# Kernel optimization log

Measured on AMD Instinct MI355X. Metric: run time of the kernel, lower is better.

The kernel has to match this reference:

```python
import jax, jax.numpy as jnp
import numpy as np

D_MODEL = 1024
NUM_HEADS = 16
D_K = D_MODEL // NUM_HEADS
CLAMP = 1e9
EPS = 1e-12


def setup_inputs() -> dict:
    key = jax.random.key(0)
    ks = jax.random.split(key, 11)
    B, S, D = 4, 2048, D_MODEL
    std = 1.0 / np.sqrt(D)
    inp = {
        'Q': jax.random.normal(ks[0], (B, S, D), jnp.float32),
        'K': jax.random.normal(ks[1], (B, S, D), jnp.float32),
        'V': jax.random.normal(ks[2], (B, S, D), jnp.float32),
        'Wq': jax.random.normal(ks[3], (D, D), jnp.float32) * std,
        'bq': jnp.zeros((D,), jnp.float32),
        'Wk': jax.random.normal(ks[4], (D, D), jnp.float32) * std,
        'bk': jnp.zeros((D,), jnp.float32),
        'Wv': jax.random.normal(ks[5], (D, D), jnp.float32) * std,
        'bv': jnp.zeros((D,), jnp.float32),
        'Wo': jax.random.normal(ks[6], (D, D), jnp.float32) * std,
        'bo': jnp.zeros((D,), jnp.float32),
    }
    return inp


def _split_heads(x):
    b, s, _ = x.shape
    return x.reshape(b, s, NUM_HEADS, D_K).transpose(0, 2, 1, 3)  # [b,h,s,dk]


def reference(Q, K, V, Wq, bq, Wk, bk, Wv, bv, Wo, bo):
    Qh = _split_heads(Q @ Wq.T + bq)
    Kh = _split_heads(K @ Wk.T + bk)
    Vh = _split_heads(V @ Wv.T + bv)
    scale = jnp.sqrt(jnp.asarray(D_K, Qh.dtype))
    scores = jnp.einsum('bhqd,bhkd->bhqk', Qh, Kh) / scale
    scores = scores - jnp.max(scores, axis=-1, keepdims=True)
    scores = jnp.clip(scores, -CLAMP, CLAMP)
    attn = jax.nn.softmax(scores, axis=-1)
    attn = jnp.clip(attn, EPS, None)
    attn = attn / jnp.sum(attn, axis=-1, keepdims=True)
    ctx = jnp.einsum('bhqk,bhkd->bhqd', attn, Vh)
    b, h, s, dk = ctx.shape
    ctx = ctx.transpose(0, 2, 1, 3).reshape(b, s, D_MODEL)
    return ctx @ Wo.T + bo
```

## Files before the change

kernel.cpp:

```cpp
#include <hip/hip_runtime.h>
#include <hip/hip_bf16.h>


typedef float  f32x4  __attribute__((ext_vector_type(4)));
typedef __bf16 bf16x8 __attribute__((ext_vector_type(8)));
typedef short  s16x8  __attribute__((ext_vector_type(8)));
typedef int    i32x4  __attribute__((ext_vector_type(4)));

#define MFMA16(a,b,c) __builtin_amdgcn_mfma_f32_16x16x32_bf16((a),(b),(c),0,0,0)

__device__ __forceinline__ unsigned short f2bf(float f) {
    union { float f; unsigned u; } v; v.f = f;
    unsigned r = v.u + 0x7fffu + ((v.u >> 16) & 1u);
    return (unsigned short)(r >> 16);
}

__device__ __forceinline__ s16x8 cvt8(const float* __restrict__ p) {
    f32x4 x = *(const f32x4*)p;
    f32x4 y = *(const f32x4*)(p + 4);
    s16x8 r;
    r[0] = (short)f2bf(x[0]); r[1] = (short)f2bf(x[1]);
    r[2] = (short)f2bf(x[2]); r[3] = (short)f2bf(x[3]);
    r[4] = (short)f2bf(y[0]); r[5] = (short)f2bf(y[1]);
    r[6] = (short)f2bf(y[2]); r[7] = (short)f2bf(y[3]);
    return r;
}

__device__ __forceinline__ void gl_lds16(const void* g, void* l) {
    __builtin_amdgcn_global_load_lds(
        (const __attribute__((address_space(1))) unsigned int*)g,
        (__attribute__((address_space(3))) unsigned int*)l, 16, 0, 0);
}

__device__ __forceinline__ float exp2_fast(float x) {
    float r;
    asm("v_exp_f32 %0, %1" : "=v"(r) : "v"(x));
    return r;
}

__device__ __forceinline__ int cvtpk_bf16(float lo, float hi) {
    int r;
    asm("v_cvt_pk_bf16_f32 %0, %1, %2" : "=v"(r) : "v"(lo), "v"(hi));
    return r;
}
__device__ __forceinline__ void plswap32(int& a, int& b) {
    asm("v_permlane32_swap_b32 %0, %1" : "+v"(a), "+v"(b));
}
__device__ __forceinline__ void plswap16(int& a, int& b) {
    asm("v_permlane16_swap_b32 %0, %1" : "+v"(a), "+v"(b));
}

__device__ __forceinline__ void pack_pf(const f32x4 pe[4], bf16x8& pf0, bf16x8& pf1) {
    int a0 = cvtpk_bf16(pe[0][0], pe[0][1]);
    int a1 = cvtpk_bf16(pe[0][2], pe[0][3]);
    int b0 = cvtpk_bf16(pe[1][0], pe[1][1]);
    int b1 = cvtpk_bf16(pe[1][2], pe[1][3]);
    plswap32(a0, b0); plswap32(a1, b1);
    plswap16(a0, b0); plswap16(a1, b1);
    i32x4 f0; f0[0] = a0; f0[1] = a1; f0[2] = b0; f0[3] = b1;
    int c0 = cvtpk_bf16(pe[2][0], pe[2][1]);
    int c1 = cvtpk_bf16(pe[2][2], pe[2][3]);
    int d0 = cvtpk_bf16(pe[3][0], pe[3][1]);
    int d1 = cvtpk_bf16(pe[3][2], pe[3][3]);
    plswap32(c0, d0); plswap32(c1, d1);
    plswap16(c0, d0); plswap16(c1, d1);
    i32x4 f1; f1[0] = c0; f1[1] = c1; f1[2] = d0; f1[3] = d1;
    pf0 = __builtin_bit_cast(bf16x8, f0);
    pf1 = __builtin_bit_cast(bf16x8, f1);
}

__global__ __launch_bounds__(256) void cvt_kernel(
    const float* __restrict__ src, unsigned short* __restrict__ dst, int n8)
{
    int i = blockIdx.x * 256 + threadIdx.x;
    if (i < n8) *(s16x8*)(dst + (size_t)i * 8) = cvt8(src + (size_t)i * 8);
}

template <int MODE>
__global__ __launch_bounds__(256) void gemm_bf16(
    const unsigned short* __restrict__ A,
    const unsigned short* __restrict__ W,
    const float* __restrict__ bias,
    void* __restrict__ Cv, float scale)
{
    constexpr int K = 1024;
    __shared__ unsigned short Ash[128 * 32];
    __shared__ unsigned short Bsh[128 * 32];

    const int t    = threadIdx.x;
    const int w    = t >> 6;
    const int lane = t & 63;
    const int wm   = w >> 1, wn = w & 1;
    const int lr   = lane & 15, quad = lane >> 4;

    const int m0 = blockIdx.y * 128;
    const int n0 = blockIdx.x * 128;

    const int srow = t >> 2;
    const int skp  = (t & 3) * 8;

    const unsigned short* Ap0 = A + (size_t)(m0 + srow) * K + skp;
    const unsigned short* Ap1 = Ap0 + (size_t)64 * K;
    const unsigned short* Wp0 = W + (size_t)(n0 + srow) * K + skp;
    const unsigned short* Wp1 = Wp0 + (size_t)64 * K;
    unsigned short* lA0 = &Ash[w * 512];
    unsigned short* lA1 = &Ash[2048 + w * 512];
    unsigned short* lB0 = &Bsh[w * 512];
    unsigned short* lB1 = &Bsh[2048 + w * 512];

    f32x4 acc[4][4] = {};

    for (int k0 = 0; k0 < K; k0 += 32) {
        __syncthreads();
        gl_lds16(Ap0 + k0, lA0);
        gl_lds16(Ap1 + k0, lA1);
        gl_lds16(Wp0 + k0, lB0);
        gl_lds16(Wp1 + k0, lB1);
        __syncthreads();

        bf16x8 af[4], bw[4];
#pragma unroll
        for (int i = 0; i < 4; i++)
            af[i] = *(const bf16x8*)&Ash[(wm * 64 + i * 16 + lr) * 32 + quad * 8];
#pragma unroll
        for (int j = 0; j < 4; j++)
            bw[j] = *(const bf16x8*)&Bsh[(wn * 64 + j * 16 + lr) * 32 + quad * 8];

#pragma unroll
        for (int i = 0; i < 4; i++)
#pragma unroll
            for (int j = 0; j < 4; j++)
                acc[i][j] = MFMA16(af[i], bw[j], acc[i][j]);
    }

#pragma unroll
    for (int i = 0; i < 4; i++) {
#pragma unroll
        for (int j = 0; j < 4; j++) {
            const int n = n0 + wn * 64 + j * 16 + lr;
#pragma unroll
            for (int r = 0; r < 4; r++) {
                const int m = m0 + wm * 64 + i * 16 + quad * 4 + r;
                float val = (acc[i][j][r] + ((MODE == 2) ? bias[m] : bias[n])) * scale;
                if (MODE == 0) {
                    const int b = m >> 11, s = m & 2047, h = n >> 6, d = n & 63;
                    ((unsigned short*)Cv)[(((size_t)(b * 16 + h) * 2048 + s) << 6) + d] = f2bf(val);
                } else if (MODE == 1) {
                    ((float*)Cv)[(size_t)m * 1024 + n] = val;
                } else {
                    const int h = m >> 6, d = m & 63, b = n >> 11, s = n & 2047;
                    ((unsigned short*)Cv)[((size_t)(b * 16 + h) * 64 + d) * 2048 + s] = f2bf(val);
                }
            }
        }
    }
}

__global__ __launch_bounds__(256) void attn_kernel(
    const unsigned short* __restrict__ Qh,
    const unsigned short* __restrict__ Kh,
    const unsigned short* __restrict__ Vt,
    unsigned short* __restrict__ ctx)
{
    constexpr int KS = 72;
    __shared__ unsigned short Ksh[64 * KS];
    __shared__ unsigned short Vts[64 * KS];

    const int t    = threadIdx.x;
    const int w    = t >> 6;
    const int lane = t & 63;
    const int lr   = lane & 15, quad = lane >> 4;

    const int bh = blockIdx.y, qblk = blockIdx.x;
    const size_t base = (size_t)bh * 2048 * 64;
    const unsigned short* Qp = Qh + base;
    const unsigned short* Kg = Kh + base + (size_t)lane * 64 + w * 16;
    const unsigned short* Vg = Vt + base + (size_t)lane * 2048 + w * 16;

    const int q0 = qblk * 128 + w * 32;
    const unsigned short* qr0 = Qp + (size_t)(q0 + lr) * 64;
    const unsigned short* qr1 = Qp + (size_t)(q0 + 16 + lr) * 64;
    bf16x8 aq0 = *(const bf16x8*)(qr0 + quad * 8);
    bf16x8 aq1 = *(const bf16x8*)(qr0 + 32 + quad * 8);
    bf16x8 aq2 = *(const bf16x8*)(qr1 + quad * 8);
    bf16x8 aq3 = *(const bf16x8*)(qr1 + 32 + quad * 8);

    f32x4 Of0[4] = {}, Of1[4] = {};
    float ls0 = 0.f, ls1 = 0.f;

    s16x8 kv0 = *(const s16x8*)(Kg);
    s16x8 kv1 = *(const s16x8*)(Kg + 8);
    s16x8 vv0 = *(const s16x8*)(Vg);
    s16x8 vv1 = *(const s16x8*)(Vg + 8);

    for (int kb = 0; kb < 2048; kb += 64) {
        __syncthreads();
        *(s16x8*)&Ksh[lane * KS + w * 16]     = kv0;
        *(s16x8*)&Ksh[lane * KS + w * 16 + 8] = kv1;
        *(s16x8*)&Vts[lane * KS + w * 16]     = vv0;
        *(s16x8*)&Vts[lane * KS + w * 16 + 8] = vv1;

        const int kn = (kb + 64) & 2047;
        kv0 = *(const s16x8*)(Kg + (size_t)kn * 64);
        kv1 = *(const s16x8*)(Kg + (size_t)kn * 64 + 8);
        vv0 = *(const s16x8*)(Vg + kn);
        vv1 = *(const s16x8*)(Vg + kn + 8);

        __syncthreads();

        f32x4 pe0[4], pe1[4];
#pragma unroll
        for (int nt = 0; nt < 4; nt++) {
            const unsigned short* kr = &Ksh[(16 * nt + lr) * KS + quad * 8];
            bf16x8 k0 = *(const bf16x8*)kr;
            bf16x8 k1 = *(const bf16x8*)(kr + 32);
            f32x4 c0 = {}, c1 = {};
            c0 = MFMA16(k0, aq0, c0); c0 = MFMA16(k1, aq1, c0);
            c1 = MFMA16(k0, aq2, c1); c1 = MFMA16(k1, aq3, c1);
            f32x4 p0, p1;
#pragma unroll
            for (int r = 0; r < 4; r++) p0[r] = exp2_fast(c0[r]);
#pragma unroll
            for (int r = 0; r < 4; r++) p1[r] = exp2_fast(c1[r]);
            ls0 += (p0[0] + p0[1]) + (p0[2] + p0[3]);
            ls1 += (p1[0] + p1[1]) + (p1[2] + p1[3]);
            pe0[nt] = p0; pe1[nt] = p1;
        }

        bf16x8 pf00, pf01, pf10, pf11;
        pack_pf(pe0, pf00, pf01);
        pack_pf(pe1, pf10, pf11);

#pragma unroll
        for (int dt = 0; dt < 4; dt++) {
            const unsigned short* vr = &Vts[(dt * 16 + lr) * KS + quad * 8];
            bf16x8 v0 = *(const bf16x8*)vr;
            bf16x8 v1 = *(const bf16x8*)(vr + 32);
            Of0[dt] = MFMA16(pf00, v0, Of0[dt]);
            Of0[dt] = MFMA16(pf01, v1, Of0[dt]);
            Of1[dt] = MFMA16(pf10, v0, Of1[dt]);
            Of1[dt] = MFMA16(pf11, v1, Of1[dt]);
        }
    }

    ls0 += __shfl_xor(ls0, 16);
    ls0 += __shfl_xor(ls0, 32);
    ls1 += __shfl_xor(ls1, 16);
    ls1 += __shfl_xor(ls1, 32);

    const int b = bh >> 4, h = bh & 15;
#pragma unroll
    for (int r = 0; r < 4; r++) {
        const float inv0 = 1.0f / __shfl(ls0, quad * 4 + r, 64);
        const int qa = q0 + quad * 4 + r;
        unsigned short* cp0 = ctx + ((size_t)b * 2048 + qa) * 1024 + h * 64;
#pragma unroll
        for (int dt = 0; dt < 4; dt++)
            cp0[dt * 16 + lr] = f2bf(Of0[dt][r] * inv0);

        const float inv1 = 1.0f / __shfl(ls1, quad * 4 + r, 64);
        const int qb = q0 + 16 + quad * 4 + r;
        unsigned short* cp1 = ctx + ((size_t)b * 2048 + qb) * 1024 + h * 64;
#pragma unroll
        for (int dt = 0; dt < 4; dt++)
            cp1[dt * 16 + lr] = f2bf(Of1[dt][r] * inv1);
    }
}

extern "C" void kernel_launch(void* const* d_in, const int* in_sizes, int n_in,
                              void* d_out, int out_size, void* d_ws, size_t ws_size,
                              hipStream_t stream) {
    const float* Q  = (const float*)d_in[0];
    const float* K  = (const float*)d_in[1];
    const float* V  = (const float*)d_in[2];
    const float* Wq = (const float*)d_in[3];
    const float* bq = (const float*)d_in[4];
    const float* Wk = (const float*)d_in[5];
    const float* bk = (const float*)d_in[6];
    const float* Wv = (const float*)d_in[7];
    const float* bv = (const float*)d_in[8];
    const float* Wo = (const float*)d_in[9];
    const float* bo = (const float*)d_in[10];

    const size_t EB = (size_t)8192 * 1024;
    const size_t EW = (size_t)1024 * 1024;
    unsigned short* Xb  = (unsigned short*)d_ws;
    unsigned short* Wqb = Xb  + EB;
    unsigned short* Wkb = Wqb + EW;
    unsigned short* Wvb = Wkb + EW;
    unsigned short* Wob = Wvb + EW;
    unsigned short* Qh  = Wob + EW;
    unsigned short* Kh  = Qh  + EB;
    unsigned short* Vtw = Kh  + EB;
    unsigned short* Ctx = Xb;

    const int n8b = (int)(EB / 8);
    const int n8w = (int)(EW / 8);

    const float QSCALE = 0.125f * 1.44269504088896340736f;

    cvt_kernel<<<n8w / 256, 256, 0, stream>>>(Wq, Wqb, n8w);
    cvt_kernel<<<n8w / 256, 256, 0, stream>>>(Wk, Wkb, n8w);
    cvt_kernel<<<n8w / 256, 256, 0, stream>>>(Wv, Wvb, n8w);
    cvt_kernel<<<n8w / 256, 256, 0, stream>>>(Wo, Wob, n8w);

    dim3 tb(256), gP(8, 64), gT(64, 8);

    cvt_kernel<<<n8b / 256, 256, 0, stream>>>(Q, Xb, n8b);
    gemm_bf16<0><<<gP, tb, 0, stream>>>(Xb, Wqb, bq, Qh, QSCALE);

    cvt_kernel<<<n8b / 256, 256, 0, stream>>>(K, Xb, n8b);
    gemm_bf16<0><<<gP, tb, 0, stream>>>(Xb, Wkb, bk, Kh, 1.0f);

    cvt_kernel<<<n8b / 256, 256, 0, stream>>>(V, Xb, n8b);
    gemm_bf16<2><<<gT, tb, 0, stream>>>(Wvb, Xb, bv, Vtw, 1.0f);

    attn_kernel<<<dim3(16, 64), tb, 0, stream>>>(Qh, Kh, Vtw, Ctx);

    gemm_bf16<1><<<gP, tb, 0, stream>>>(Ctx, Wob, bo, (float*)d_out, 1.0f);
}
```

Baseline: 373.0 us.

## Double-buffer GEMM LDS tiles, remap block order, fuse weight conversions

The GEMM now double-buffers its LDS tiles. It issues the next k-slice's global-to-LDS loads before computing the current one and waits with explicit vmcnt counts, so the load of one slice overlaps the MFMAs of the previous one. For the non-transposed modes, the block index is remapped so consecutive blocks share the same N-column of weights, which should help L2 reuse. The four weight-conversion launches are merged into one kernel. LDS use per block doubles, which may reduce occupancy, and correctness depends on the hand-written waitcnt and barrier placement.

```diff
diff --git a/kernel.cpp b/kernel.cpp
--- a/kernel.cpp
+++ b/kernel.cpp
@@ -76,6 +76,19 @@
     if (i < n8) *(s16x8*)(dst + (size_t)i * 8) = cvt8(src + (size_t)i * 8);
 }
 
+__global__ __launch_bounds__(256) void wcvt_kernel(
+    const float* __restrict__ s0, const float* __restrict__ s1,
+    const float* __restrict__ s2, const float* __restrict__ s3,
+    unsigned short* __restrict__ d0, unsigned short* __restrict__ d1,
+    unsigned short* __restrict__ d2, unsigned short* __restrict__ d3)
+{
+    const int which = blockIdx.x >> 9;
+    const int i = (blockIdx.x & 511) * 256 + threadIdx.x;
+    const float* s = (which == 0) ? s0 : (which == 1) ? s1 : (which == 2) ? s2 : s3;
+    unsigned short* d = (which == 0) ? d0 : (which == 1) ? d1 : (which == 2) ? d2 : d3;
+    *(s16x8*)(d + (size_t)i * 8) = cvt8(s + (size_t)i * 8);
+}
+
 template <int MODE>
 __global__ __launch_bounds__(256) void gemm_bf16(
     const unsigned short* __restrict__ A,
@@ -84,8 +97,8 @@
     void* __restrict__ Cv, float scale)
 {
     constexpr int K = 1024;
-    __shared__ unsigned short Ash[128 * 32];
-    __shared__ unsigned short Bsh[128 * 32];
+    __shared__ unsigned short Ash[2 * 128 * 32];
+    __shared__ unsigned short Bsh[2 * 128 * 32];
 
     const int t    = threadIdx.x;
     const int w    = t >> 6;
@@ -93,8 +106,16 @@
     const int wm   = w >> 1, wn = w & 1;
     const int lr   = lane & 15, quad = lane >> 4;
 
-    const int m0 = blockIdx.y * 128;
-    const int n0 = blockIdx.x * 128;
+    int m0, n0;
+    if (MODE == 2) {
+        m0 = blockIdx.y * 128;
+        n0 = blockIdx.x * 128;
+    } else {
+        const int bid  = blockIdx.y * 8 + blockIdx.x;
+        const int orig = (bid & 7) * 64 + (bid >> 3);
+        n0 = (orig & 7) * 128;
+        m0 = (orig >> 3) * 128;
+    }
 
     const int srow = t >> 2;
     const int skp  = (t & 3) * 8;
@@ -108,30 +129,47 @@
     unsigned short* lB0 = &Bsh[w * 512];
     unsigned short* lB1 = &Bsh[2048 + w * 512];
 
+#define STAGE(buf, k0) do {                       \
+        gl_lds16(Ap0 + (k0), lA0 + (buf) * 4096); \
+        gl_lds16(Ap1 + (k0), lA1 + (buf) * 4096); \
+        gl_lds16(Wp0 + (k0), lB0 + (buf) * 4096); \
+        gl_lds16(Wp1 + (k0), lB1 + (buf) * 4096); \
+    } while (0)
+
     f32x4 acc[4][4] = {};
 
+    STAGE(0, 0);
+    int cur = 0;
+
     for (int k0 = 0; k0 < K; k0 += 32) {
-        __syncthreads();
-        gl_lds16(Ap0 + k0, lA0);
-        gl_lds16(Ap1 + k0, lA1);
-        gl_lds16(Wp0 + k0, lB0);
-        gl_lds16(Wp1 + k0, lB1);
-        __syncthreads();
+        if (k0 + 32 < K) {
+            STAGE(cur ^ 1, k0 + 32);
+            asm volatile("s_waitcnt vmcnt(4)" ::: "memory");
+        } else {
+            asm volatile("s_waitcnt vmcnt(0)" ::: "memory");
+        }
+        __builtin_amdgcn_s_barrier();
+        __builtin_amdgcn_sched_barrier(0);
 
         bf16x8 af[4], bw[4];
 #pragma unroll
         for (int i = 0; i < 4; i++)
-            af[i] = *(const bf16x8*)&Ash[(wm * 64 + i * 16 + lr) * 32 + quad * 8];
+            af[i] = *(const bf16x8*)&Ash[cur * 4096 + (wm * 64 + i * 16 + lr) * 32 + quad * 8];
 #pragma unroll
         for (int j = 0; j < 4; j++)
-            bw[j] = *(const bf16x8*)&Bsh[(wn * 64 + j * 16 + lr) * 32 + quad * 8];
+            bw[j] = *(const bf16x8*)&Bsh[cur * 4096 + (wn * 64 + j * 16 + lr) * 32 + quad * 8];
 
 #pragma unroll
         for (int i = 0; i < 4; i++)
 #pragma unroll
             for (int j = 0; j < 4; j++)
                 acc[i][j] = MFMA16(af[i], bw[j], acc[i][j]);
-    }
+
+        __builtin_amdgcn_sched_barrier(0);
+        __builtin_amdgcn_s_barrier();
+        cur ^= 1;
+    }
+#undef STAGE
 
 #pragma unroll
     for (int i = 0; i < 4; i++) {
@@ -295,14 +333,10 @@
     unsigned short* Ctx = Xb;
 
     const int n8b = (int)(EB / 8);
-    const int n8w = (int)(EW / 8);
 
     const float QSCALE = 0.125f * 1.44269504088896340736f;
 
-    cvt_kernel<<<n8w / 256, 256, 0, stream>>>(Wq, Wqb, n8w);
-    cvt_kernel<<<n8w / 256, 256, 0, stream>>>(Wk, Wkb, n8w);
-    cvt_kernel<<<n8w / 256, 256, 0, stream>>>(Wv, Wvb, n8w);
-    cvt_kernel<<<n8w / 256, 256, 0, stream>>>(Wo, Wob, n8w);
+    wcvt_kernel<<<2048, 256, 0, stream>>>(Wq, Wk, Wv, Wo, Wqb, Wkb, Wvb, Wob);
 
     dim3 tb(256), gP(8, 64), gT(64, 8);
 
```

After: 358.3 us. -4.0%, faster.

## Fuse fp32-to-bf16 conversion into projection GEMMs and batch QKV in one launch

Applied to the files above, without the earlier changes.

Removes the separate conversion kernels for inputs and weights. The GEMMs now load fp32 directly, convert to bf16 in registers and store to LDS, with register prefetch of the next k-tile. The three QKV projections run as one launch over grid z, and the block index mapping is swizzled so that blocks sharing the same A rows run together. This saves the extra bf16 write and read passes and many launches, but each GEMM now reads twice the global bytes per tile and adds conversion ALU work in place of async global-to-LDS loads.

```diff
diff --git a/kernel.cpp b/kernel.cpp
--- a/kernel.cpp
+++ b/kernel.cpp
@@ -15,23 +15,6 @@
     return (unsigned short)(r >> 16);
 }
 
-__device__ __forceinline__ s16x8 cvt8(const float* __restrict__ p) {
-    f32x4 x = *(const f32x4*)p;
-    f32x4 y = *(const f32x4*)(p + 4);
-    s16x8 r;
-    r[0] = (short)f2bf(x[0]); r[1] = (short)f2bf(x[1]);
-    r[2] = (short)f2bf(x[2]); r[3] = (short)f2bf(x[3]);
-    r[4] = (short)f2bf(y[0]); r[5] = (short)f2bf(y[1]);
-    r[6] = (short)f2bf(y[2]); r[7] = (short)f2bf(y[3]);
-    return r;
-}
-
-__device__ __forceinline__ void gl_lds16(const void* g, void* l) {
-    __builtin_amdgcn_global_load_lds(
-        (const __attribute__((address_space(1))) unsigned int*)g,
-        (__attribute__((address_space(3))) unsigned int*)l, 16, 0, 0);
-}
-
 __device__ __forceinline__ float exp2_fast(float x) {
     float r;
     asm("v_exp_f32 %0, %1" : "=v"(r) : "v"(x));
@@ -42,6 +25,14 @@
     int r;
     asm("v_cvt_pk_bf16_f32 %0, %1, %2" : "=v"(r) : "v"(lo), "v"(hi));
     return r;
+}
+__device__ __forceinline__ s16x8 pk8(f32x4 x, f32x4 y) {
+    i32x4 r;
+    r[0] = cvtpk_bf16(x[0], x[1]);
+    r[1] = cvtpk_bf16(x[2], x[3]);
+    r[2] = cvtpk_bf16(y[0], y[1]);
+    r[3] = cvtpk_bf16(y[2], y[3]);
+    return __builtin_bit_cast(s16x8, r);
 }
 __device__ __forceinline__ void plswap32(int& a, int& b) {
     asm("v_permlane32_swap_b32 %0, %1" : "+v"(a), "+v"(b));
@@ -69,19 +60,15 @@
     pf1 = __builtin_bit_cast(bf16x8, f1);
 }
 
-__global__ __launch_bounds__(256) void cvt_kernel(
-    const float* __restrict__ src, unsigned short* __restrict__ dst, int n8)
-{
-    int i = blockIdx.x * 256 + threadIdx.x;
-    if (i < n8) *(s16x8*)(dst + (size_t)i * 8) = cvt8(src + (size_t)i * 8);
-}
-
-template <int MODE>
-__global__ __launch_bounds__(256) void gemm_bf16(
-    const unsigned short* __restrict__ A,
-    const unsigned short* __restrict__ W,
-    const float* __restrict__ bias,
-    void* __restrict__ Cv, float scale)
+__global__ __launch_bounds__(256) void proj_kernel(
+    const float* __restrict__ Qf, const float* __restrict__ Kf,
+    const float* __restrict__ Vf,
+    const float* __restrict__ Wqf, const float* __restrict__ Wkf,
+    const float* __restrict__ Wvf,
+    const float* __restrict__ bqf, const float* __restrict__ bkf,
+    const float* __restrict__ bvf,
+    unsigned short* __restrict__ Qh, unsigned short* __restrict__ Kh,
+    unsigned short* __restrict__ Vtw, float qscale)
 {
     constexpr int K = 1024;
     __shared__ unsigned short Ash[128 * 32];
@@ -93,29 +80,140 @@
     const int wm   = w >> 1, wn = w & 1;
     const int lr   = lane & 15, quad = lane >> 4;
 
-    const int m0 = blockIdx.y * 128;
-    const int n0 = blockIdx.x * 128;
+    const int z = blockIdx.z;
+    const float *Af, *Wf, *bias;
+    float scale;
+    unsigned short* out;
+    if (z == 0)      { Af = Qf;  Wf = Wqf; bias = bqf; out = Qh;  scale = qscale; }
+    else if (z == 1) { Af = Kf;  Wf = Wkf; bias = bkf; out = Kh;  scale = 1.0f; }
+    else             { Af = Wvf; Wf = Vf;  bias = bvf; out = Vtw; scale = 1.0f; }
+
+    int m0, n0;
+    if (z < 2) {
+        m0 = (blockIdx.x * 8 + (blockIdx.y >> 3)) * 128;
+        n0 = (blockIdx.y & 7) * 128;
+    } else {
+        m0 = (blockIdx.y & 7) * 128;
+        n0 = (blockIdx.x * 8 + (blockIdx.y >> 3)) * 128;
+    }
 
     const int srow = t >> 2;
     const int skp  = (t & 3) * 8;
 
+    const float* Ap0 = Af + (size_t)(m0 + srow) * K + skp;
+    const float* Ap1 = Ap0 + (size_t)64 * K;
+    const float* Wp0 = Wf + (size_t)(n0 + srow) * K + skp;
+    const float* Wp1 = Wp0 + (size_t)64 * K;
+    unsigned short* dA = &Ash[srow * 32 + skp];
+    unsigned short* dB = &Bsh[srow * 32 + skp];
+
+    f32x4 a0x, a0y, a1x, a1y, w0x, w0y, w1x, w1y;
+#define LOADP(kk) do {                                                        \
+        a0x = *(const f32x4*)(Ap0 + (kk)); a0y = *(const f32x4*)(Ap0 + (kk) + 4); \
+        a1x = *(const f32x4*)(Ap1 + (kk)); a1y = *(const f32x4*)(Ap1 + (kk) + 4); \
+        w0x = *(const f32x4*)(Wp0 + (kk)); w0y = *(const f32x4*)(Wp0 + (kk) + 4); \
+        w1x = *(const f32x4*)(Wp1 + (kk)); w1y = *(const f32x4*)(Wp1 + (kk) + 4); \
+    } while (0)
+
+    f32x4 acc[4][4] = {};
+    LOADP(0);
+
+    for (int k0 = 0; k0 < K; k0 += 32) {
+        __syncthreads();
+        *(s16x8*)dA              = pk8(a0x, a0y);
+        *(s16x8*)(dA + 64 * 32)  = pk8(a1x, a1y);
+        *(s16x8*)dB              = pk8(w0x, w0y);
+        *(s16x8*)(dB + 64 * 32)  = pk8(w1x, w1y);
+        const int kn = (k0 + 32) & 1023;
+        LOADP(kn);
+        __syncthreads();
+
+        bf16x8 af[4], bw[4];
+#pragma unroll
+        for (int i = 0; i < 4; i++)
+            af[i] = *(const bf16x8*)&Ash[(wm * 64 + i * 16 + lr) * 32 + quad * 8];
+#pragma unroll
+        for (int j = 0; j < 4; j++)
+            bw[j] = *(const bf16x8*)&Bsh[(wn * 64 + j * 16 + lr) * 32 + quad * 8];
+
+#pragma unroll
+        for (int i = 0; i < 4; i++)
+#pragma unroll
+            for (int j = 0; j < 4; j++)
+                acc[i][j] = MFMA16(af[i], bw[j], acc[i][j]);
+    }
+#undef LOADP
+
+#pragma unroll
+    for (int i = 0; i < 4; i++) {
+#pragma unroll
+        for (int j = 0; j < 4; j++) {
+            const int n = n0 + wn * 64 + j * 16 + lr;
+#pragma unroll
+            for (int r = 0; r < 4; r++) {
+                const int m = m0 + wm * 64 + i * 16 + quad * 4 + r;
+                float val = (acc[i][j][r] + ((z == 2) ? bias[m] : bias[n])) * scale;
+                if (z < 2) {
+                    const int b = m >> 11, s = m & 2047, h = n >> 6, d = n & 63;
+                    out[(((size_t)(b * 16 + h) * 2048 + s) << 6) + d] = f2bf(val);
+                } else {
+                    const int h = m >> 6, d = m & 63, b = n >> 11, s = n & 2047;
+                    out[((size_t)(b * 16 + h) * 64 + d) * 2048 + s] = f2bf(val);
+                }
+            }
+        }
+    }
+}
+
+__global__ __launch_bounds__(256) void gemm_o(
+    const unsigned short* __restrict__ A,
+    const float* __restrict__ Wf,
+    const float* __restrict__ bias,
+    float* __restrict__ out)
+{
+    constexpr int K = 1024;
+    __shared__ unsigned short Ash[128 * 32];
+    __shared__ unsigned short Bsh[128 * 32];
+
+    const int t    = threadIdx.x;
+    const int w    = t >> 6;
+    const int lane = t & 63;
+    const int wm   = w >> 1, wn = w & 1;
+    const int lr   = lane & 15, quad = lane >> 4;
+
+    const int m0 = (blockIdx.x * 8 + (blockIdx.y >> 3)) * 128;
+    const int n0 = (blockIdx.y & 7) * 128;
+
+    const int srow = t >> 2;
+    const int skp  = (t & 3) * 8;
+
     const unsigned short* Ap0 = A + (size_t)(m0 + srow) * K + skp;
     const unsigned short* Ap1 = Ap0 + (size_t)64 * K;
-    const unsigned short* Wp0 = W + (size_t)(n0 + srow) * K + skp;
-    const unsigned short* Wp1 = Wp0 + (size_t)64 * K;
-    unsigned short* lA0 = &Ash[w * 512];
-    unsigned short* lA1 = &Ash[2048 + w * 512];
-    unsigned short* lB0 = &Bsh[w * 512];
-    unsigned short* lB1 = &Bsh[2048 + w * 512];
+    const float* Wp0 = Wf + (size_t)(n0 + srow) * K + skp;
+    const float* Wp1 = Wp0 + (size_t)64 * K;
+    unsigned short* dA = &Ash[srow * 32 + skp];
+    unsigned short* dB = &Bsh[srow * 32 + skp];
+
+    s16x8 av0, av1;
+    f32x4 w0x, w0y, w1x, w1y;
+#define LOADO(kk) do {                                                        \
+        av0 = *(const s16x8*)(Ap0 + (kk));                                    \
+        av1 = *(const s16x8*)(Ap1 + (kk));                                    \
+        w0x = *(const f32x4*)(Wp0 + (kk)); w0y = *(const f32x4*)(Wp0 + (kk) + 4); \
+        w1x = *(const f32x4*)(Wp1 + (kk)); w1y = *(const f32x4*)(Wp1 + (kk) + 4); \
+    } while (0)
 
     f32x4 acc[4][4] = {};
+    LOADO(0);
 
     for (int k0 = 0; k0 < K; k0 += 32) {
         __syncthreads();
-        gl_lds16(Ap0 + k0, lA0);
-        gl_lds16(Ap1 + k0, lA1);
-        gl_lds16(Wp0 + k0, lB0);
-        gl_lds16(Wp1 + k0, lB1);
+        *(s16x8*)dA             = av0;
+        *(s16x8*)(dA + 64 * 32) = av1;
+        *(s16x8*)dB             = pk8(w0x, w0y);
+        *(s16x8*)(dB + 64 * 32) = pk8(w1x, w1y);
+        const int kn = (k0 + 32) & 1023;
+        LOADO(kn);
         __syncthreads();
 
         bf16x8 af[4], bw[4];
@@ -132,6 +230,7 @@
             for (int j = 0; j < 4; j++)
                 acc[i][j] = MFMA16(af[i], bw[j], acc[i][j]);
     }
+#undef LOADO
 
 #pragma unroll
     for (int i = 0; i < 4; i++) {
@@ -141,16 +240,7 @@
 #pragma unroll
             for (int r = 0; r < 4; r++) {
                 const int m = m0 + wm * 64 + i * 16 + quad * 4 + r;
-                float val = (acc[i][j][r] + ((MODE == 2) ? bias[m] : bias[n])) * scale;
-                if (MODE == 0) {
-                    const int b = m >> 11, s = m & 2047, h = n >> 6, d = n & 63;
-                    ((unsigned short*)Cv)[(((size_t)(b * 16 + h) * 2048 + s) << 6) + d] = f2bf(val);
-                } else if (MODE == 1) {
-                    ((float*)Cv)[(size_t)m * 1024 + n] = val;
-                } else {
-                    const int h = m >> 6, d = m & 63, b = n >> 11, s = n & 2047;
-                    ((unsigned short*)Cv)[((size_t)(b * 16 + h) * 64 + d) * 2048 + s] = f2bf(val);
-                }
+                out[(size_t)m * 1024 + n] = acc[i][j][r] + bias[n];
             }
         }
     }
@@ -283,39 +373,16 @@
     const float* bo = (const float*)d_in[10];
 
     const size_t EB = (size_t)8192 * 1024;
-    const size_t EW = (size_t)1024 * 1024;
-    unsigned short* Xb  = (unsigned short*)d_ws;
-    unsigned short* Wqb = Xb  + EB;
-    unsigned short* Wkb = Wqb + EW;
-    unsigned short* Wvb = Wkb + EW;
-    unsigned short* Wob = Wvb + EW;
-    unsigned short* Qh  = Wob + EW;
+    unsigned short* Qh  = (unsigned short*)d_ws;
     unsigned short* Kh  = Qh  + EB;
     unsigned short* Vtw = Kh  + EB;
-    unsigned short* Ctx = Xb;
-
-    const int n8b = (int)(EB / 8);
-    const int n8w = (int)(EW / 8);
+    unsigned short* Ctx = Vtw + EB;
 
     const float QSCALE = 0.125f * 1.44269504088896340736f;
 
-    cvt_kernel<<<n8w / 256, 256, 0, stream>>>(Wq, Wqb, n8w);
-    cvt_kernel<<<n8w / 256, 256, 0, stream>>>(Wk, Wkb, n8w);
-    cvt_kernel<<<n8w / 256, 256, 0, stream>>>(Wv, Wvb, n8w);
-    cvt_kernel<<<n8w / 256, 256, 0, stream>>>(Wo, Wob, n8w);
-
-    dim3 tb(256), gP(8, 64), gT(64, 8);
-
-    cvt_kernel<<<n8b / 256, 256, 0, stream>>>(Q, Xb, n8b);
-    gemm_bf16<0><<<gP, tb, 0, stream>>>(Xb, Wqb, bq, Qh, QSCALE);
-
-    cvt_kernel<<<n8b / 256, 256, 0, stream>>>(K, Xb, n8b);
-    gemm_bf16<0><<<gP, tb, 0, stream>>>(Xb, Wkb, bk, Kh, 1.0f);
-
-    cvt_kernel<<<n8b / 256, 256, 0, stream>>>(V, Xb, n8b);
-    gemm_bf16<2><<<gT, tb, 0, stream>>>(Wvb, Xb, bv, Vtw, 1.0f);
-
+    dim3 tb(256);
+    proj_kernel<<<dim3(8, 64, 3), tb, 0, stream>>>(
+        Q, K, V, Wq, Wk, Wv, bq, bk, bv, Qh, Kh, Vtw, QSCALE);
     attn_kernel<<<dim3(16, 64), tb, 0, stream>>>(Qh, Kh, Vtw, Ctx);
-
-    gemm_bf16<1><<<gP, tb, 0, stream>>>(Ctx, Wob, bo, (float*)d_out, 1.0f);
-}
+    gemm_o<<<dim3(8, 64), tb, 0, stream>>>(Ctx, Wo, bo, (float*)d_out);
+}
```

After: 384.4 us. 3.1% more time.
